# Performance work log

Hardware: AMD Instinct MI355X
Metric: run time of the kernel (lower is better)

The kernel has to match this reference:

```python
import jax, jax.numpy as jnp
import numpy as np

BOUNDS = [0.01, 1.0, 100.0]
STEPS = [128, 128]
ALPHA_C = 0.01          # cfg.renderer.alpha
N_IMPORTANCE = 128      # cfg.renderer.importance_steps
N_RAYS = 65536


def _zvals_log_coarse():
    # matches torch.linspace(log10(b[i]), log10(b[i+1]) - seg/steps[i], steps[i]) per segment
    segs = []
    for i, s in enumerate(STEPS):
        lo = np.log10(BOUNDS[i]); hi = np.log10(BOUNDS[i + 1])
        segs.append(np.linspace(lo, hi - (hi - lo) / s, s, dtype=np.float32))
    return np.concatenate(segs)


def _seg_scale():
    tot = float(sum(STEPS))
    return np.concatenate([np.full(s, s / tot, dtype=np.float32) for s in STEPS])


def setup_inputs() -> dict:
    key = jax.random.key(0)
    k1, k2, k3, k4 = jax.random.split(key, 4)
    sigmas_coarse = jax.random.uniform(k1, (N_RAYS, sum(STEPS)), dtype=jnp.float32) * 5.0
    sigmas_fine = jax.random.uniform(k2, (N_RAYS, N_IMPORTANCE), dtype=jnp.float32) * 5.0
    rgbs_fine = jax.random.uniform(k3, (N_RAYS, N_IMPORTANCE, 3), dtype=jnp.float32)
    bg_color = jax.random.uniform(k4, (3,), dtype=jnp.float32)
    return {"sigmas_coarse": sigmas_coarse, "sigmas_fine": sigmas_fine,
            "rgbs_fine": rgbs_fine, "bg_color": bg_color}


def _weights_from_sigmas(sigmas, z_log):
    # delta[:, :-1] = diff(z_log), last delta = 0 (as in efficient_sampling)
    delta = jnp.concatenate([z_log[:, 1:] - z_log[:, :-1], jnp.zeros_like(z_log[:, :1])], -1)
    alpha = 1.0 - jnp.exp(-sigmas * delta)
    alpha_shift = jnp.concatenate([jnp.zeros_like(alpha[:, :1]), alpha[:, :-1]], -1)
    trans = jnp.cumprod(1.0 - alpha_shift, axis=-1)   # transmittance
    return alpha * trans


def _reweight(weights):
    # pad with zeros, 3-tap max blur, floor by alpha/S, per-segment rescale, normalize
    wpad = jnp.pad(weights, ((0, 0), (1, 1)))
    w = 0.5 * (jnp.maximum(wpad[:, :-2], wpad[:, 1:-1]) + jnp.maximum(wpad[:, 1:-1], wpad[:, 2:]))
    w = w + ALPHA_C / w.shape[-1]
    w = w * jnp.asarray(_seg_scale())
    return w / jnp.sum(w, axis=-1, keepdims=True)


def _sample_pdf(bins, weights, n_samples):
    # weights already normalized -> pdf; deterministic stratified u for reproducibility
    cdf = jnp.cumsum(weights, axis=-1)                     # [N, S]
    u = (jnp.arange(n_samples, dtype=bins.dtype) + 0.5) / n_samples
    u = jnp.broadcast_to(u, (bins.shape[0], n_samples))    # [N, n]
    inds = jax.vmap(lambda c, uu: jnp.searchsorted(c, uu, side='right'))(cdf, u)
    S = bins.shape[-1]
    below = jnp.clip(inds - 1, 0, S - 1)
    above = jnp.clip(inds, 0, S - 1)
    cdf_b = jnp.take_along_axis(cdf, below, -1)
    cdf_a = jnp.take_along_axis(cdf, above, -1)
    bin_b = jnp.take_along_axis(bins, below, -1)
    bin_a = jnp.take_along_axis(bins, above, -1)
    denom = jnp.where(cdf_a - cdf_b < 1e-5, 1.0, cdf_a - cdf_b)
    t = (u - cdf_b) / denom
    return bin_b + t * (bin_a - bin_b)


def reference(sigmas_coarse, sigmas_fine, rgbs_fine, bg_color):
    # --- efficient_sampling (no_grad path) ---
    z_log = jnp.broadcast_to(jnp.asarray(_zvals_log_coarse()), sigmas_coarse.shape)
    w_coarse = _weights_from_sigmas(sigmas_coarse, z_log)
    w_re = _reweight(w_coarse)
    z_log_fine = _sample_pdf(z_log, w_re, N_IMPORTANCE)     # [N, n_imp], sorted
    z_fine = jnp.power(10.0, z_log_fine)
    # --- render_rays_log-style compositing on fine samples ---
    w_fine = _weights_from_sigmas(sigmas_fine, z_log_fine)
    image = jnp.einsum('ns,nsc->nc', w_fine, rgbs_fine)
    image = image + (1.0 - jnp.sum(w_fine, -1)[..., None]) * bg_color
    invdepth = jnp.sum(w_fine / z_fine, axis=-1)
    lo = np.float32(np.log10(BOUNDS[0])); hi = np.float32(np.log10(BOUNDS[-1]))
    z_log_s = (z_log_fine - lo) / (hi - lo)
    return image, invdepth, w_fine, z_log_s
```

## Files before the change

### kernel.cpp

```cpp
#include <hip/hip_runtime.h>

#define SC 256
#define NF 128

template<int CTRL, int RM, int BM>
__device__ __forceinline__ float dpp_add(float x) {
    int s = __builtin_amdgcn_update_dpp(0, __float_as_int(x), CTRL, RM, BM, true);
    return x + __int_as_float(s);
}
template<int CTRL>
__device__ __forceinline__ float dpp_mov0(float x) {
    return __int_as_float(__builtin_amdgcn_update_dpp(0, __float_as_int(x), CTRL, 0xF, 0xF, true));
}
__device__ __forceinline__ float lane_f(float x, int l) {
    return __int_as_float(__builtin_amdgcn_readlane(__float_as_int(x), l));
}

__device__ __forceinline__ float wave_incl_scan(float x) {
    x = dpp_add<0x111, 0xF, 0xF>(x);
    x = dpp_add<0x112, 0xF, 0xF>(x);
    x = dpp_add<0x114, 0xF, 0xF>(x);
    x = dpp_add<0x118, 0xF, 0xF>(x);
    x = dpp_add<0x142, 0xA, 0xF>(x);
    x = dpp_add<0x143, 0xC, 0xF>(x);
    return x;
}

__device__ __forceinline__ float wave_sum_lane0(float x) {
    x = dpp_add<0xB1, 0xF, 0xF>(x);
    x = dpp_add<0x4E, 0xF, 0xF>(x);
    x = dpp_add<0x124, 0xF, 0xF>(x);
    x = dpp_add<0x128, 0xF, 0xF>(x);
    return x + lane_f(x, 16) + lane_f(x, 32) + lane_f(x, 48);
}

__global__ __launch_bounds__(256) void nerf_render_kernel(
    const float* __restrict__ sig_c,
    const float* __restrict__ sig_f,
    const float* __restrict__ rgb_f,
    const float* __restrict__ bg,
    float* __restrict__ out,
    int n_rays)
{
    const int lane = threadIdx.x & 63;
    const int wid  = threadIdx.x >> 6;
    const int ray  = (blockIdx.x << 2) + wid;
    if (ray >= n_rays) return;

    __shared__ float s_cdf[4][SC];

    const float4 sc4 = *reinterpret_cast<const float4*>(sig_c + (size_t)ray * SC + 4 * lane);
    const float DLT = 0.015625f;
    float x0 = sc4.x * DLT;
    float x1 = sc4.y * DLT;
    float x2 = sc4.z * DLT;
    float x3 = (lane == 63) ? 0.0f : sc4.w * DLT;

    float p0 = x0, p1 = p0 + x1, p2 = p1 + x2, p3 = p2 + x3;
    float incl = wave_incl_scan(p3);
    float excl = incl - p3;

    float T0 = __expf(-excl);
    float T1 = __expf(-(excl + p0));
    float T2 = __expf(-(excl + p1));
    float T3 = __expf(-(excl + p2));
    float T4 = __expf(-(excl + p3));
    float w0 = T0 - T1, w1 = T1 - T2, w2 = T2 - T3, w3 = T3 - T4;

    float wl = dpp_mov0<0x138>(w3);
    float wr = dpp_mov0<0x130>(w0);

    const float FLOOR = 0.01f / 256.0f;
    float m01 = fmaxf(w0, w1), m12 = fmaxf(w1, w2), m23 = fmaxf(w2, w3);
    float r0 = 0.5f * (fmaxf(wl, w0) + m01) + FLOOR;
    float r1 = 0.5f * (m01 + m12) + FLOOR;
    float r2 = 0.5f * (m12 + m23) + FLOOR;
    float r3 = 0.5f * (m23 + fmaxf(w3, wr)) + FLOOR;

    float q0 = r0, q1 = q0 + r1, q2 = q1 + r2, q3 = q2 + r3;
    float incl2 = wave_incl_scan(q3);
    float excl2 = incl2 - q3;
    float total = lane_f(incl2, 63);
    float inv_total = __builtin_amdgcn_rcpf(total);

    *reinterpret_cast<float4*>(&s_cdf[wid][4 * lane]) = make_float4(
        (excl2 + q0) * inv_total, (excl2 + q1) * inv_total,
        (excl2 + q2) * inv_total, (excl2 + q3) * inv_total);

    __syncthreads();

    const float* cdf = s_cdf[wid];
    float zl[2];
    #pragma unroll
    for (int s = 0; s < 2; ++s) {
        const int k = 2 * lane + s;
        const float u = ((float)k + 0.5f) * (1.0f / 128.0f);
        int pos = 0;
        #pragma unroll
        for (int step = 128; step >= 1; step >>= 1) {
            if (cdf[pos + step - 1] <= u) pos += step;
        }
        int below = pos - 1; if (below < 0) below = 0;
        int above = pos;     if (above > SC - 1) above = SC - 1;
        float cdf_b = cdf[below];
        float cdf_a = cdf[above];
        float bin_b = -2.0f + (float)below * 0.015625f;
        float bin_a = -2.0f + (float)above * 0.015625f;
        float dn = cdf_a - cdf_b;
        dn = (dn < 1e-5f) ? 1.0f : dn;
        float t = (u - cdf_b) / dn;
        zl[s] = bin_b + t * (bin_a - bin_b);
    }
    float zl0 = zl[0], zl1 = zl[1];

    float znext = dpp_mov0<0x130>(zl0);
    float d0 = zl1 - zl0;
    float d1 = (lane == 63) ? 0.0f : (znext - zl1);

    const float2 sf = *reinterpret_cast<const float2*>(sig_f + (size_t)ray * NF + 2 * lane);
    float y0 = sf.x * d0;
    float y1 = sf.y * d1;
    float ps = y0 + y1;
    float fincl = wave_incl_scan(ps);
    float fexcl = fincl - ps;

    float U0 = __expf(-fexcl);
    float U1 = __expf(-(fexcl + y0));
    float U2 = __expf(-(fexcl + ps));
    float wf0 = U0 - U1, wf1 = U1 - U2;

    const float2* rp = reinterpret_cast<const float2*>(rgb_f + (size_t)ray * (NF * 3) + 6 * lane);
    float2 ra = rp[0], rb = rp[1], rc = rp[2];
    float img_r = wf0 * ra.x + wf1 * rb.y;
    float img_g = wf0 * ra.y + wf1 * rc.x;
    float img_b = wf0 * rb.x + wf1 * rc.y;
    float wsum  = wf0 + wf1;
    float invd = wf0 * __exp10f(-zl0) + wf1 * __exp10f(-zl1);

    img_r = wave_sum_lane0(img_r);
    img_g = wave_sum_lane0(img_g);
    img_b = wave_sum_lane0(img_b);
    wsum  = wave_sum_lane0(wsum);
    invd  = wave_sum_lane0(invd);

    float* out_img  = out;
    float* out_invd = out + (size_t)n_rays * 3;
    float* out_wf   = out + (size_t)n_rays * 4;
    float* out_zs   = out + (size_t)n_rays * 4 + (size_t)n_rays * NF;

    if (lane == 0) {
        float one_m = 1.0f - wsum;
        out_img[(size_t)ray * 3 + 0] = img_r + one_m * bg[0];
        out_img[(size_t)ray * 3 + 1] = img_g + one_m * bg[1];
        out_img[(size_t)ray * 3 + 2] = img_b + one_m * bg[2];
        out_invd[ray] = invd;
    }
    *reinterpret_cast<float2*>(out_wf + (size_t)ray * NF + 2 * lane) =
        make_float2(wf0, wf1);
    *reinterpret_cast<float2*>(out_zs + (size_t)ray * NF + 2 * lane) =
        make_float2((zl0 + 2.0f) * 0.25f, (zl1 + 2.0f) * 0.25f);
}

extern "C" void kernel_launch(void* const* d_in, const int* in_sizes, int n_in,
                              void* d_out, int out_size, void* d_ws, size_t ws_size,
                              hipStream_t stream) {
    const float* sig_c = (const float*)d_in[0];
    const float* sig_f = (const float*)d_in[1];
    const float* rgb_f = (const float*)d_in[2];
    const float* bg    = (const float*)d_in[3];
    float* out = (float*)d_out;

    const int n_rays = in_sizes[1] / NF;
    dim3 grid((n_rays + 3) / 4), block(256);
    hipLaunchKernelGGL(nerf_render_kernel, grid, block, 0, stream,
                       sig_c, sig_f, rgb_f, bg, out, n_rays);
}
```

Baseline: 232.6 us.

## Replace per-sample binary search with scatter from CDF bins and hoist global loads

Each lane now walks its own four CDF bins and writes the interpolated fine sample positions for every stratified u that falls in each bin straight into shared memory, in place of running an eight-step binary search per sample. The block-wide __syncthreads is replaced by an lgkmcnt wait, since each wave only reads its own row. Loads of the fine sigmas, RGB values and background colour are moved to the start of the kernel so they overlap with the coarse computation, and launch bounds now request higher occupancy. The per-bin loop has a data-dependent trip count, which causes divergence within a wave, and the interpolation and edge clamping differ slightly from the reference search.

```diff
diff --git a/kernel.cpp b/kernel.cpp
--- a/kernel.cpp
+++ b/kernel.cpp
@@ -34,7 +34,13 @@
     return x + lane_f(x, 16) + lane_f(x, 32) + lane_f(x, 48);
 }
 
-__global__ __launch_bounds__(256) void nerf_render_kernel(
+__device__ __forceinline__ int Kfun(float c) {
+    float g = 128.0f * c - 0.5f;
+    int k = (int)ceilf(g);
+    return k < 0 ? 0 : (k > NF ? NF : k);
+}
+
+__global__ __launch_bounds__(256, 8) void nerf_render_kernel(
     const float* __restrict__ sig_c,
     const float* __restrict__ sig_f,
     const float* __restrict__ rgb_f,
@@ -47,9 +53,14 @@
     const int ray  = (blockIdx.x << 2) + wid;
     if (ray >= n_rays) return;
 
-    __shared__ float s_cdf[4][SC];
+    __shared__ float s_z[4][NF];
 
     const float4 sc4 = *reinterpret_cast<const float4*>(sig_c + (size_t)ray * SC + 4 * lane);
+    const float2 sf  = *reinterpret_cast<const float2*>(sig_f + (size_t)ray * NF + 2 * lane);
+    const float2* rp = reinterpret_cast<const float2*>(rgb_f + (size_t)ray * (NF * 3) + 6 * lane);
+    const float2 ra = rp[0], rb = rp[1], rc = rp[2];
+    const float bg0 = bg[0], bg1 = bg[1], bg2 = bg[2];
+
     const float DLT = 0.015625f;
     float x0 = sc4.x * DLT;
     float x1 = sc4.y * DLT;
@@ -83,41 +94,42 @@
     float total = lane_f(incl2, 63);
     float inv_total = __builtin_amdgcn_rcpf(total);
 
-    *reinterpret_cast<float4*>(&s_cdf[wid][4 * lane]) = make_float4(
-        (excl2 + q0) * inv_total, (excl2 + q1) * inv_total,
-        (excl2 + q2) * inv_total, (excl2 + q3) * inv_total);
+    float c0 = (excl2 + q0) * inv_total;
+    float c1 = (excl2 + q1) * inv_total;
+    float c2 = (excl2 + q2) * inv_total;
+    float c3 = (excl2 + q3) * inv_total;
+    float cprev = dpp_mov0<0x138>(c3);
 
-    __syncthreads();
+    float* row = s_z[wid];
+    {
+        float cs[4] = {c0, c1, c2, c3};
+        float cm = cprev;
+        int   Km = Kfun(cprev);
+        #pragma unroll
+        for (int m = 0; m < 4; ++m) {
+            float cn = cs[m];
+            int   Kn = (lane == 63 && m == 3) ? NF : Kfun(cn);
+            int   bin = 4 * lane + m;
+            float zb = -2.0f + (float)(bin - 1) * DLT;
+            float slope = DLT * __builtin_amdgcn_rcpf(cn - cm);
+            for (int k = Km; k < Kn; ++k) {
+                float u = ((float)k + 0.5f) * 0.0078125f;
+                float z = (bin == 0) ? -2.0f : fmaf(u - cm, slope, zb);
+                row[k] = z;
+            }
+            cm = cn; Km = Kn;
+        }
+    }
 
-    const float* cdf = s_cdf[wid];
-    float zl[2];
-    #pragma unroll
-    for (int s = 0; s < 2; ++s) {
-        const int k = 2 * lane + s;
-        const float u = ((float)k + 0.5f) * (1.0f / 128.0f);
-        int pos = 0;
-        #pragma unroll
-        for (int step = 128; step >= 1; step >>= 1) {
-            if (cdf[pos + step - 1] <= u) pos += step;
-        }
-        int below = pos - 1; if (below < 0) below = 0;
-        int above = pos;     if (above > SC - 1) above = SC - 1;
-        float cdf_b = cdf[below];
-        float cdf_a = cdf[above];
-        float bin_b = -2.0f + (float)below * 0.015625f;
-        float bin_a = -2.0f + (float)above * 0.015625f;
-        float dn = cdf_a - cdf_b;
-        dn = (dn < 1e-5f) ? 1.0f : dn;
-        float t = (u - cdf_b) / dn;
-        zl[s] = bin_b + t * (bin_a - bin_b);
-    }
-    float zl0 = zl[0], zl1 = zl[1];
+    __asm__ volatile("s_waitcnt lgkmcnt(0)" ::: "memory");
+
+    float2 zl2 = *reinterpret_cast<const float2*>(&row[2 * lane]);
+    float zl0 = zl2.x, zl1 = zl2.y;
 
     float znext = dpp_mov0<0x130>(zl0);
     float d0 = zl1 - zl0;
     float d1 = (lane == 63) ? 0.0f : (znext - zl1);
 
-    const float2 sf = *reinterpret_cast<const float2*>(sig_f + (size_t)ray * NF + 2 * lane);
     float y0 = sf.x * d0;
     float y1 = sf.y * d1;
     float ps = y0 + y1;
@@ -129,13 +141,11 @@
     float U2 = __expf(-(fexcl + ps));
     float wf0 = U0 - U1, wf1 = U1 - U2;
 
-    const float2* rp = reinterpret_cast<const float2*>(rgb_f + (size_t)ray * (NF * 3) + 6 * lane);
-    float2 ra = rp[0], rb = rp[1], rc = rp[2];
     float img_r = wf0 * ra.x + wf1 * rb.y;
     float img_g = wf0 * ra.y + wf1 * rc.x;
     float img_b = wf0 * rb.x + wf1 * rc.y;
     float wsum  = wf0 + wf1;
-    float invd = wf0 * __exp10f(-zl0) + wf1 * __exp10f(-zl1);
+    float invd  = wf0 * __exp10f(-zl0) + wf1 * __exp10f(-zl1);
 
     img_r = wave_sum_lane0(img_r);
     img_g = wave_sum_lane0(img_g);
@@ -150,9 +160,9 @@
 
     if (lane == 0) {
         float one_m = 1.0f - wsum;
-        out_img[(size_t)ray * 3 + 0] = img_r + one_m * bg[0];
-        out_img[(size_t)ray * 3 + 1] = img_g + one_m * bg[1];
-        out_img[(size_t)ray * 3 + 2] = img_b + one_m * bg[2];
+        out_img[(size_t)ray * 3 + 0] = img_r + one_m * bg0;
+        out_img[(size_t)ray * 3 + 1] = img_g + one_m * bg1;
+        out_img[(size_t)ray * 3 + 2] = img_b + one_m * bg2;
         out_invd[ray] = invd;
     }
     *reinterpret_cast<float2*>(out_wf + (size_t)ray * NF + 2 * lane) =
```

After: 238.0 us. +2.3%, slower.

## Use persistent waves with register prefetch of next ray's inputs

Applied to the files above, without the earlier changes.

Replaces the one-ray-per-wave launch with a fixed grid of 2048 blocks. Each wave loops over rays with a stride of the total wave count and loads the next ray's sigma and rgb inputs into registers while computing the current ray. It also swaps __syncthreads for a per-wave lgkmcnt wait, uses nontemporal stores for the large per-sample outputs, and sets launch bounds for 8 blocks. The aim is to overlap global load latency with compute and cut block launch overhead, at the cost of higher register pressure and a fixed grid size.

```diff
diff --git a/kernel.cpp b/kernel.cpp
--- a/kernel.cpp
+++ b/kernel.cpp
@@ -2,6 +2,10 @@
 
 #define SC 256
 #define NF 128
+#define NBLOCKS 2048
+#define NWAVES (NBLOCKS * 4)
+
+typedef float v2f __attribute__((ext_vector_type(2)));
 
 template<int CTRL, int RM, int BM>
 __device__ __forceinline__ float dpp_add(float x) {
@@ -34,7 +38,7 @@
     return x + lane_f(x, 16) + lane_f(x, 32) + lane_f(x, 48);
 }
 
-__global__ __launch_bounds__(256) void nerf_render_kernel(
+__global__ __launch_bounds__(256, 8) void nerf_render_kernel(
     const float* __restrict__ sig_c,
     const float* __restrict__ sig_f,
     const float* __restrict__ rgb_f,
@@ -44,121 +48,141 @@
 {
     const int lane = threadIdx.x & 63;
     const int wid  = threadIdx.x >> 6;
-    const int ray  = (blockIdx.x << 2) + wid;
-    if (ray >= n_rays) return;
+    const int wave = (blockIdx.x << 2) + wid;
 
     __shared__ float s_cdf[4][SC];
-
-    const float4 sc4 = *reinterpret_cast<const float4*>(sig_c + (size_t)ray * SC + 4 * lane);
-    const float DLT = 0.015625f;
-    float x0 = sc4.x * DLT;
-    float x1 = sc4.y * DLT;
-    float x2 = sc4.z * DLT;
-    float x3 = (lane == 63) ? 0.0f : sc4.w * DLT;
-
-    float p0 = x0, p1 = p0 + x1, p2 = p1 + x2, p3 = p2 + x3;
-    float incl = wave_incl_scan(p3);
-    float excl = incl - p3;
-
-    float T0 = __expf(-excl);
-    float T1 = __expf(-(excl + p0));
-    float T2 = __expf(-(excl + p1));
-    float T3 = __expf(-(excl + p2));
-    float T4 = __expf(-(excl + p3));
-    float w0 = T0 - T1, w1 = T1 - T2, w2 = T2 - T3, w3 = T3 - T4;
-
-    float wl = dpp_mov0<0x138>(w3);
-    float wr = dpp_mov0<0x130>(w0);
-
-    const float FLOOR = 0.01f / 256.0f;
-    float m01 = fmaxf(w0, w1), m12 = fmaxf(w1, w2), m23 = fmaxf(w2, w3);
-    float r0 = 0.5f * (fmaxf(wl, w0) + m01) + FLOOR;
-    float r1 = 0.5f * (m01 + m12) + FLOOR;
-    float r2 = 0.5f * (m12 + m23) + FLOOR;
-    float r3 = 0.5f * (m23 + fmaxf(w3, wr)) + FLOOR;
-
-    float q0 = r0, q1 = q0 + r1, q2 = q1 + r2, q3 = q2 + r3;
-    float incl2 = wave_incl_scan(q3);
-    float excl2 = incl2 - q3;
-    float total = lane_f(incl2, 63);
-    float inv_total = __builtin_amdgcn_rcpf(total);
-
-    *reinterpret_cast<float4*>(&s_cdf[wid][4 * lane]) = make_float4(
-        (excl2 + q0) * inv_total, (excl2 + q1) * inv_total,
-        (excl2 + q2) * inv_total, (excl2 + q3) * inv_total);
-
-    __syncthreads();
-
-    const float* cdf = s_cdf[wid];
-    float zl[2];
-    #pragma unroll
-    for (int s = 0; s < 2; ++s) {
-        const int k = 2 * lane + s;
-        const float u = ((float)k + 0.5f) * (1.0f / 128.0f);
-        int pos = 0;
-        #pragma unroll
-        for (int step = 128; step >= 1; step >>= 1) {
-            if (cdf[pos + step - 1] <= u) pos += step;
-        }
-        int below = pos - 1; if (below < 0) below = 0;
-        int above = pos;     if (above > SC - 1) above = SC - 1;
-        float cdf_b = cdf[below];
-        float cdf_a = cdf[above];
-        float bin_b = -2.0f + (float)below * 0.015625f;
-        float bin_a = -2.0f + (float)above * 0.015625f;
-        float dn = cdf_a - cdf_b;
-        dn = (dn < 1e-5f) ? 1.0f : dn;
-        float t = (u - cdf_b) / dn;
-        zl[s] = bin_b + t * (bin_a - bin_b);
-    }
-    float zl0 = zl[0], zl1 = zl[1];
-
-    float znext = dpp_mov0<0x130>(zl0);
-    float d0 = zl1 - zl0;
-    float d1 = (lane == 63) ? 0.0f : (znext - zl1);
-
-    const float2 sf = *reinterpret_cast<const float2*>(sig_f + (size_t)ray * NF + 2 * lane);
-    float y0 = sf.x * d0;
-    float y1 = sf.y * d1;
-    float ps = y0 + y1;
-    float fincl = wave_incl_scan(ps);
-    float fexcl = fincl - ps;
-
-    float U0 = __expf(-fexcl);
-    float U1 = __expf(-(fexcl + y0));
-    float U2 = __expf(-(fexcl + ps));
-    float wf0 = U0 - U1, wf1 = U1 - U2;
-
-    const float2* rp = reinterpret_cast<const float2*>(rgb_f + (size_t)ray * (NF * 3) + 6 * lane);
-    float2 ra = rp[0], rb = rp[1], rc = rp[2];
-    float img_r = wf0 * ra.x + wf1 * rb.y;
-    float img_g = wf0 * ra.y + wf1 * rc.x;
-    float img_b = wf0 * rb.x + wf1 * rc.y;
-    float wsum  = wf0 + wf1;
-    float invd = wf0 * __exp10f(-zl0) + wf1 * __exp10f(-zl1);
-
-    img_r = wave_sum_lane0(img_r);
-    img_g = wave_sum_lane0(img_g);
-    img_b = wave_sum_lane0(img_b);
-    wsum  = wave_sum_lane0(wsum);
-    invd  = wave_sum_lane0(invd);
+    float* cdf = s_cdf[wid];
+
+    const float bg0 = bg[0], bg1 = bg[1], bg2 = bg[2];
 
     float* out_img  = out;
     float* out_invd = out + (size_t)n_rays * 3;
     float* out_wf   = out + (size_t)n_rays * 4;
     float* out_zs   = out + (size_t)n_rays * 4 + (size_t)n_rays * NF;
 
-    if (lane == 0) {
-        float one_m = 1.0f - wsum;
-        out_img[(size_t)ray * 3 + 0] = img_r + one_m * bg[0];
-        out_img[(size_t)ray * 3 + 1] = img_g + one_m * bg[1];
-        out_img[(size_t)ray * 3 + 2] = img_b + one_m * bg[2];
-        out_invd[ray] = invd;
+    const int niter = (n_rays + NWAVES - 1) / NWAVES;
+
+    int ray = wave;
+    int rc0 = ray < n_rays ? ray : n_rays - 1;
+    float4 sc4 = *reinterpret_cast<const float4*>(sig_c + (size_t)rc0 * SC + 4 * lane);
+    float2 sf  = *reinterpret_cast<const float2*>(sig_f + (size_t)rc0 * NF + 2 * lane);
+    const float2* rp = reinterpret_cast<const float2*>(rgb_f + (size_t)rc0 * (NF * 3) + 6 * lane);
+    float2 ra = rp[0], rb = rp[1], rc = rp[2];
+
+    for (int it = 0; it < niter; ++it) {
+        int ray_n = ray + NWAVES;
+        int rcn = ray_n < n_rays ? ray_n : n_rays - 1;
+        float4 nsc = *reinterpret_cast<const float4*>(sig_c + (size_t)rcn * SC + 4 * lane);
+        float2 nsf = *reinterpret_cast<const float2*>(sig_f + (size_t)rcn * NF + 2 * lane);
+        const float2* nrp = reinterpret_cast<const float2*>(rgb_f + (size_t)rcn * (NF * 3) + 6 * lane);
+        float2 nra = nrp[0], nrb = nrp[1], nrc = nrp[2];
+
+        const float DLT = 0.015625f;
+        float x0 = sc4.x * DLT;
+        float x1 = sc4.y * DLT;
+        float x2 = sc4.z * DLT;
+        float x3 = (lane == 63) ? 0.0f : sc4.w * DLT;
+
+        float p0 = x0, p1 = p0 + x1, p2 = p1 + x2, p3 = p2 + x3;
+        float incl = wave_incl_scan(p3);
+        float excl = incl - p3;
+
+        float T0 = __expf(-excl);
+        float T1 = __expf(-(excl + p0));
+        float T2 = __expf(-(excl + p1));
+        float T3 = __expf(-(excl + p2));
+        float T4 = __expf(-(excl + p3));
+        float w0 = T0 - T1, w1 = T1 - T2, w2 = T2 - T3, w3 = T3 - T4;
+
+        float wl = dpp_mov0<0x138>(w3);
+        float wr = dpp_mov0<0x130>(w0);
+
+        const float FLOOR = 0.01f / 256.0f;
+        float m01 = fmaxf(w0, w1), m12 = fmaxf(w1, w2), m23 = fmaxf(w2, w3);
+        float r0 = 0.5f * (fmaxf(wl, w0) + m01) + FLOOR;
+        float r1 = 0.5f * (m01 + m12) + FLOOR;
+        float r2 = 0.5f * (m12 + m23) + FLOOR;
+        float r3 = 0.5f * (m23 + fmaxf(w3, wr)) + FLOOR;
+
+        float q0 = r0, q1 = q0 + r1, q2 = q1 + r2, q3 = q2 + r3;
+        float incl2 = wave_incl_scan(q3);
+        float excl2 = incl2 - q3;
+        float total = lane_f(incl2, 63);
+        float inv_total = __builtin_amdgcn_rcpf(total);
+
+        *reinterpret_cast<float4*>(&cdf[4 * lane]) = make_float4(
+            (excl2 + q0) * inv_total, (excl2 + q1) * inv_total,
+            (excl2 + q2) * inv_total, (excl2 + q3) * inv_total);
+
+        __asm__ volatile("s_waitcnt lgkmcnt(0)" ::: "memory");
+
+        float zl[2];
+        #pragma unroll
+        for (int s = 0; s < 2; ++s) {
+            const int k = 2 * lane + s;
+            const float u = ((float)k + 0.5f) * (1.0f / 128.0f);
+            int pos = 0;
+            #pragma unroll
+            for (int step = 128; step >= 1; step >>= 1) {
+                if (cdf[pos + step - 1] <= u) pos += step;
+            }
+            int below = pos - 1; if (below < 0) below = 0;
+            int above = pos;     if (above > SC - 1) above = SC - 1;
+            float cdf_b = cdf[below];
+            float cdf_a = cdf[above];
+            float bin_b = -2.0f + (float)below * DLT;
+            float bin_a = -2.0f + (float)above * DLT;
+            float dn = cdf_a - cdf_b;
+            dn = (dn < 1e-5f) ? 1.0f : dn;
+            float t = (u - cdf_b) / dn;
+            zl[s] = bin_b + t * (bin_a - bin_b);
+        }
+        float zl0 = zl[0], zl1 = zl[1];
+
+        float znext = dpp_mov0<0x130>(zl0);
+        float d0 = zl1 - zl0;
+        float d1 = (lane == 63) ? 0.0f : (znext - zl1);
+
+        float y0 = sf.x * d0;
+        float y1 = sf.y * d1;
+        float ps = y0 + y1;
+        float fincl = wave_incl_scan(ps);
+        float fexcl = fincl - ps;
+
+        float U0 = __expf(-fexcl);
+        float U1 = __expf(-(fexcl + y0));
+        float U2 = __expf(-(fexcl + ps));
+        float wf0 = U0 - U1, wf1 = U1 - U2;
+
+        float img_r = wf0 * ra.x + wf1 * rb.y;
+        float img_g = wf0 * ra.y + wf1 * rc.x;
+        float img_b = wf0 * rb.x + wf1 * rc.y;
+        float wsum  = wf0 + wf1;
+        float invd  = wf0 * __exp10f(-zl0) + wf1 * __exp10f(-zl1);
+
+        img_r = wave_sum_lane0(img_r);
+        img_g = wave_sum_lane0(img_g);
+        img_b = wave_sum_lane0(img_b);
+        wsum  = wave_sum_lane0(wsum);
+        invd  = wave_sum_lane0(invd);
+
+        if (ray < n_rays) {
+            if (lane == 0) {
+                float one_m = 1.0f - wsum;
+                out_img[(size_t)ray * 3 + 0] = img_r + one_m * bg0;
+                out_img[(size_t)ray * 3 + 1] = img_g + one_m * bg1;
+                out_img[(size_t)ray * 3 + 2] = img_b + one_m * bg2;
+                out_invd[ray] = invd;
+            }
+            v2f vwf; vwf.x = wf0; vwf.y = wf1;
+            v2f vzs; vzs.x = (zl0 + 2.0f) * 0.25f; vzs.y = (zl1 + 2.0f) * 0.25f;
+            __builtin_nontemporal_store(vwf, (v2f*)(out_wf + (size_t)ray * NF + 2 * lane));
+            __builtin_nontemporal_store(vzs, (v2f*)(out_zs + (size_t)ray * NF + 2 * lane));
+        }
+
+        sc4 = nsc; sf = nsf; ra = nra; rb = nrb; rc = nrc;
+        ray = ray_n;
     }
-    *reinterpret_cast<float2*>(out_wf + (size_t)ray * NF + 2 * lane) =
-        make_float2(wf0, wf1);
-    *reinterpret_cast<float2*>(out_zs + (size_t)ray * NF + 2 * lane) =
-        make_float2((zl0 + 2.0f) * 0.25f, (zl1 + 2.0f) * 0.25f);
 }
 
 extern "C" void kernel_launch(void* const* d_in, const int* in_sizes, int n_in,
@@ -171,7 +195,7 @@
     float* out = (float*)d_out;
 
     const int n_rays = in_sizes[1] / NF;
-    dim3 grid((n_rays + 3) / 4), block(256);
+    dim3 grid(NBLOCKS), block(256);
     hipLaunchKernelGGL(nerf_render_kernel, grid, block, 0, stream,
                        sig_c, sig_f, rgb_f, bg, out, n_rays);
 }
```

After: 246.6 us. 6.0% more time.
